# Performance work log

Measured on AMD Instinct MI355X. Metric: run time of the kernel, lower is better.

The kernel has to match this reference:

```python
import jax, jax.numpy as jnp
import numpy as np

D_MODEL = 1024
NUM_HEADS = 16
D_K = D_MODEL // NUM_HEADS


def setup_inputs() -> dict:
    key = jax.random.key(0)
    ks = jax.random.split(key, 9)
    B, S = 2, 2048
    s_in = 1.0 / np.sqrt(D_MODEL)
    x = jax.random.normal(ks[0], (B, S, D_MODEL), dtype=jnp.float32)
    # Linear weights stored as (in_features, out_features): y = x @ W + b
    Wq = jax.random.uniform(ks[1], (D_MODEL, D_MODEL), jnp.float32, -s_in, s_in)
    bq = jax.random.uniform(ks[2], (D_MODEL,), jnp.float32, -s_in, s_in)
    Wk = jax.random.uniform(ks[3], (D_MODEL, D_K), jnp.float32, -s_in, s_in)
    bk = jax.random.uniform(ks[4], (D_K,), jnp.float32, -s_in, s_in)
    Wv = jax.random.uniform(ks[5], (D_MODEL, D_K), jnp.float32, -s_in, s_in)
    bv = jax.random.uniform(ks[6], (D_K,), jnp.float32, -s_in, s_in)
    Wo = jax.random.uniform(ks[7], (D_MODEL, D_MODEL), jnp.float32, -s_in, s_in)
    bo = jax.random.uniform(ks[8], (D_MODEL,), jnp.float32, -s_in, s_in)
    return {"x": x, "Wq": Wq, "bq": bq, "Wk": Wk, "bk": bk,
            "Wv": Wv, "bv": bv, "Wo": Wo, "bo": bo}


def reference(x, Wq, bq, Wk, bk, Wv, bv, Wo, bo):
    B, S, _ = x.shape
    H, Dk = NUM_HEADS, D_K
    # Projections
    Q = (x @ Wq + bq).reshape(B, S, H, Dk).transpose(0, 2, 1, 3)  # [B,H,S,Dk]
    K = x @ Wk + bk                                               # [B,S,Dk] single KV head
    V = x @ Wv + bv                                               # [B,S,Dk]
    # Scores: query heads broadcast against the single shared KV head
    scores = jnp.einsum('bhqd,bkd->bhqk', Q, K) / jnp.sqrt(jnp.float32(Dk))
    attn = jax.nn.softmax(scores, axis=-1)                        # [B,H,S,S]
    out = jnp.einsum('bhqk,bkd->bhqd', attn, V)                   # [B,H,S,Dk]
    out = out.transpose(0, 2, 1, 3).reshape(B, S, H * Dk)         # [B,S,d_model]
    return out @ Wo + bo
```

## Files before the change

kernel.cpp:

```cpp
#include <hip/hip_runtime.h>
#include <hip/hip_bf16.h>

typedef __attribute__((ext_vector_type(8))) short bf16x8;
typedef __attribute__((ext_vector_type(4))) float f32x4;
typedef __attribute__((ext_vector_type(16))) float f32x16;
typedef __attribute__((ext_vector_type(4))) unsigned short ushort4v;

#define QSCALE 0.1803368801111204f

__device__ __forceinline__ unsigned short f2bf(float f) {
  union { float f; unsigned int u; } x; x.f = f;
  unsigned int u = x.u;
  unsigned int r = (u + 0x7fffu + ((u >> 16) & 1u)) >> 16;
  return (unsigned short)r;
}

__device__ __forceinline__ void gll16(const unsigned short* g, unsigned short* l) {
  __builtin_amdgcn_global_load_lds(
      (const __attribute__((address_space(1))) unsigned int*)g,
      (__attribute__((address_space(3))) unsigned int*)l, 16, 0, 0);
}

__global__ __launch_bounds__(256) void prep_kernel(
    const float* __restrict__ x,
    const float* __restrict__ Wq, const float* __restrict__ Wk,
    const float* __restrict__ Wv, const float* __restrict__ Wo,
    unsigned short* __restrict__ xb,
    unsigned short* __restrict__ QKVt, unsigned short* __restrict__ Wot) {
  int z = blockIdx.z;
  if (z == 4) {
    size_t base = ((size_t)(blockIdx.y * 32 + blockIdx.x)) * 4096 + threadIdx.x * 16;
#pragma unroll
    for (int c = 0; c < 4; ++c) {
      float4 v = *(const float4*)(x + base + c * 4);
      ushort4v o = { f2bf(v.x), f2bf(v.y), f2bf(v.z), f2bf(v.w) };
      *(ushort4v*)(xb + base + c * 4) = o;
    }
    return;
  }
  __shared__ float t[32][33];
  const float* src;
  unsigned short* dst;
  int C, rowoff;
  if (z == 0)      { src = Wq; dst = QKVt; C = 1024; rowoff = 0; }
  else if (z == 1) { src = Wk; dst = QKVt; C = 64;   rowoff = 1024; }
  else if (z == 2) { src = Wv; dst = QKVt; C = 64;   rowoff = 1088; }
  else             { src = Wo; dst = Wot;  C = 1024; rowoff = 0; }
  int c0 = blockIdx.x * 32, r0 = blockIdx.y * 32;
  if (c0 >= C) return;
  int tx = threadIdx.x & 31, ty = threadIdx.x >> 5;
#pragma unroll
  for (int i = 0; i < 32; i += 8)
    t[ty + i][tx] = src[(size_t)(r0 + ty + i) * C + c0 + tx];
  __syncthreads();
#pragma unroll
  for (int i = 0; i < 32; i += 8)
    dst[(size_t)(rowoff + c0 + ty + i) * 1024 + r0 + tx] = f2bf(t[tx][ty + i]);
}

template <typename OutT, bool QKVMODE>
__global__ __launch_bounds__(256, 4) void gemm_bf16_kernel(
    const unsigned short* __restrict__ A, const unsigned short* __restrict__ Bt,
    const float* __restrict__ b0, const float* __restrict__ b1,
    const float* __restrict__ b2, OutT* __restrict__ C,
    unsigned short* __restrict__ Vt, int M, int N, int K) {
  __shared__ __align__(16) unsigned short As[2][64 * 32];
  __shared__ __align__(16) unsigned short Bs[2][64 * 32];
  int tid = threadIdx.x;
  int wid = tid >> 6, lane = tid & 63;
  int l15 = lane & 15, quad = lane >> 4;
  int m0 = blockIdx.x * 64, n0 = blockIdx.y * 64;
  int mw = (wid >> 1) * 32, nw = (wid & 1) * 32;
  f32x4 acc[2][2];
#pragma unroll
  for (int i = 0; i < 2; i++)
#pragma unroll
    for (int j = 0; j < 2; j++)
#pragma unroll
      for (int e = 0; e < 4; ++e) acc[i][j][e] = 0.f;

  int u = tid;
  int srow = u >> 2;
  int gq = (u & 3) ^ ((srow >> 1) & 3);
  const unsigned short* Ag = A + (size_t)(m0 + srow) * K + gq * 8;
  const unsigned short* Bg = Bt + (size_t)(n0 + srow) * K + gq * 8;

  gll16(Ag, As[0] + u * 8);
  gll16(Bg, Bs[0] + u * 8);

  for (int k0 = 0; k0 < K; k0 += 32) {
    int cur = (k0 >> 5) & 1;
    if (k0 + 32 < K) {
      int nxt = cur ^ 1;
      gll16(Ag + k0 + 32, As[nxt] + u * 8);
      gll16(Bg + k0 + 32, Bs[nxt] + u * 8);
      asm volatile("s_waitcnt vmcnt(2)" ::: "memory");
    } else {
      asm volatile("s_waitcnt vmcnt(0)" ::: "memory");
    }
    __builtin_amdgcn_s_barrier();
    __builtin_amdgcn_sched_barrier(0);
    const unsigned short* Asb = As[cur];
    const unsigned short* Bsb = Bs[cur];
    bf16x8 af[2], bfr[2];
#pragma unroll
    for (int t = 0; t < 2; ++t) {
      int row = mw + t * 16 + l15;
      af[t] = *(const bf16x8*)(Asb + row * 32 + ((quad ^ ((row >> 1) & 3)) * 8));
    }
#pragma unroll
    for (int t = 0; t < 2; ++t) {
      int row = nw + t * 16 + l15;
      bfr[t] = *(const bf16x8*)(Bsb + row * 32 + ((quad ^ ((row >> 1) & 3)) * 8));
    }
#pragma unroll
    for (int mt = 0; mt < 2; ++mt)
#pragma unroll
      for (int nt = 0; nt < 2; ++nt)
        acc[mt][nt] = __builtin_amdgcn_mfma_f32_16x16x32_bf16(
            af[mt], bfr[nt], acc[mt][nt], 0, 0, 0);
    asm volatile("s_waitcnt lgkmcnt(0)" ::: "memory");
    __builtin_amdgcn_sched_barrier(0);
    __builtin_amdgcn_s_barrier();
  }
#pragma unroll
  for (int mt = 0; mt < 2; ++mt)
#pragma unroll
    for (int nt = 0; nt < 2; ++nt) {
      int col = n0 + nw + nt * 16 + l15;
      float bias, cs;
      if constexpr (QKVMODE) {
        bias = (col < 1024) ? b0[col] : ((col < 1088) ? b1[col - 1024] : b2[col - 1088]);
        cs = (col < 1024) ? QSCALE : 1.0f;
      } else {
        bias = b0[col];
        cs = 1.0f;
      }
#pragma unroll
      for (int r = 0; r < 4; ++r) {
        int row = m0 + mw + mt * 16 + quad * 4 + r;
        float v = (acc[mt][nt][r] + bias) * cs;
        if constexpr (sizeof(OutT) == 2)
          C[(size_t)row * N + col] = f2bf(v);
        else
          C[(size_t)row * N + col] = v;
        if constexpr (QKVMODE) {
          if (col >= 1088)
            Vt[((size_t)(row >> 11) * 64 + (col - 1088)) * 2048 + (row & 2047)] =
                f2bf(v);
        }
      }
    }
}

__global__ __launch_bounds__(512, 4) void flash_attn_kernel(
    const unsigned short* __restrict__ QKV,
    const unsigned short* __restrict__ Vt,
    unsigned short* __restrict__ AO) {
  constexpr int S = 2048, LDQ = 1152;
  constexpr int PK = 72;
  __shared__ __align__(16) unsigned short smem[2][2][64 * PK];
  int tid = threadIdx.x;
  int wid = tid >> 6, lane = tid & 63;
  int l31 = lane & 31, half = lane >> 5;
  int p = wid & 3, ks = wid >> 2;
  int q0 = blockIdx.x * 128, h = blockIdx.y, b = blockIdx.z;

  const unsigned short* Qb =
      QKV + (size_t)(b * S + q0 + p * 32 + l31) * LDQ + h * 64 + half * 8;
  bf16x8 qf[4];
#pragma unroll
  for (int f = 0; f < 4; ++f) qf[f] = *(const bf16x8*)(Qb + f * 16);

  int u = tid & 255, sl = tid >> 8;
  int srow = u >> 2, sc = (u & 3) * 8;
  const unsigned short* Kgb = QKV + ((size_t)b * S) * LDQ + 1024;
  const unsigned short* Vgb = Vt + ((size_t)(b * 64 + srow)) * 2048;

  f32x16 oa0, oa1;
#pragma unroll
  for (int r = 0; r < 16; ++r) { oa0[r] = 0.f; oa1[r] = 0.f; }
  float rs = 0.f;

  int kb0 = sl * 1024;
  bf16x8 ka = *(const bf16x8*)(Kgb + (size_t)(kb0 + srow) * LDQ + sc);
  bf16x8 kc = *(const bf16x8*)(Kgb + (size_t)(kb0 + srow) * LDQ + sc + 32);
  bf16x8 va = *(const bf16x8*)(Vgb + kb0 + sc);
  bf16x8 vc = *(const bf16x8*)(Vgb + kb0 + sc + 32);

  unsigned short* Ksb = smem[ks][0];
  unsigned short* Vsb = smem[ks][1];

  for (int kt = 0; kt < 16; ++kt) {
    *(bf16x8*)(smem[sl][0] + srow * PK + sc) = ka;
    *(bf16x8*)(smem[sl][0] + srow * PK + sc + 32) = kc;
    *(bf16x8*)(smem[sl][1] + srow * PK + sc) = va;
    *(bf16x8*)(smem[sl][1] + srow * PK + sc + 32) = vc;
    __syncthreads();
    if (kt + 1 < 16) {
      int kbn = sl * 1024 + (kt + 1) * 64;
      ka = *(const bf16x8*)(Kgb + (size_t)(kbn + srow) * LDQ + sc);
      kc = *(const bf16x8*)(Kgb + (size_t)(kbn + srow) * LDQ + sc + 32);
      va = *(const bf16x8*)(Vgb + kbn + sc);
      vc = *(const bf16x8*)(Vgb + kbn + sc + 32);
    }

#pragma unroll
    for (int n2 = 0; n2 < 2; ++n2) {
      f32x16 sacc;
#pragma unroll
      for (int i = 0; i < 16; ++i) sacc[i] = 0.f;
#pragma unroll
      for (int s = 0; s < 4; ++s) {
        bf16x8 kf =
            *(const bf16x8*)(Ksb + (n2 * 32 + l31) * PK + s * 16 + half * 8);
        sacc = __builtin_amdgcn_mfma_f32_32x32x16_bf16(kf, qf[s], sacc, 0, 0, 0);
      }
#pragma unroll
      for (int t = 0; t < 2; ++t) {
        float pr[8];
#pragma unroll
        for (int j = 0; j < 8; ++j) {
          pr[j] = __builtin_amdgcn_exp2f(sacc[t * 8 + j]);
          rs += pr[j];
        }
        unsigned w0A, w1A, w0B, w1B;
        asm("v_cvt_pk_bf16_f32 %0, %1, %2" : "=v"(w0A) : "v"(pr[0]), "v"(pr[1]));
        asm("v_cvt_pk_bf16_f32 %0, %1, %2" : "=v"(w1A) : "v"(pr[2]), "v"(pr[3]));
        asm("v_cvt_pk_bf16_f32 %0, %1, %2" : "=v"(w0B) : "v"(pr[4]), "v"(pr[5]));
        asm("v_cvt_pk_bf16_f32 %0, %1, %2" : "=v"(w1B) : "v"(pr[6]), "v"(pr[7]));
        asm volatile("v_permlane32_swap_b32 %0, %1" : "+v"(w0A), "+v"(w0B));
        asm volatile("v_permlane32_swap_b32 %0, %1" : "+v"(w1A), "+v"(w1B));
        union { unsigned u[4]; bf16x8 v; } afu;
        afu.u[0] = w0A; afu.u[1] = w1A; afu.u[2] = w0B; afu.u[3] = w1B;
        int sg = n2 * 2 + t;
        bf16x8 vf0 = *(const bf16x8*)(Vsb + (l31) * PK + sg * 16 + half * 8);
        bf16x8 vf1 = *(const bf16x8*)(Vsb + (32 + l31) * PK + sg * 16 + half * 8);
        oa0 = __builtin_amdgcn_mfma_f32_32x32x16_bf16(afu.v, vf0, oa0, 0, 0, 0);
        oa1 = __builtin_amdgcn_mfma_f32_32x32x16_bf16(afu.v, vf1, oa1, 0, 0, 0);
      }
    }
    __syncthreads();
  }

  float rsf = rs + __shfl_xor(rs, 32, 64);

  float* Cb = (float*)smem;
  if (ks == 1) {
#pragma unroll
    for (int r = 0; r < 16; ++r) {
      int row = (r & 3) + 8 * (r >> 2) + 4 * half;
      Cb[(p * 32 + row) * 66 + l31] = oa0[r];
      Cb[(p * 32 + row) * 66 + 32 + l31] = oa1[r];
    }
    if (half == 0) Cb[(p * 32 + l31) * 66 + 64] = rsf;
  } else {
    if (half == 0) Cb[(p * 32 + l31) * 66 + 65] = rsf;
  }
  __syncthreads();
  if (ks == 0) {
    unsigned short* Ob = AO + (size_t)(b * S + q0 + p * 32) * 1024 + h * 64;
#pragma unroll
    for (int r = 0; r < 16; ++r) {
      int row = (r & 3) + 8 * (r >> 2) + 4 * half;
      float p0 = Cb[(p * 32 + row) * 66 + l31];
      float p1 = Cb[(p * 32 + row) * 66 + 32 + l31];
      float inv = 1.0f / (Cb[(p * 32 + row) * 66 + 64] + Cb[(p * 32 + row) * 66 + 65]);
      Ob[(size_t)row * 1024 + l31] = f2bf((oa0[r] + p0) * inv);
      Ob[(size_t)row * 1024 + 32 + l31] = f2bf((oa1[r] + p1) * inv);
    }
  }
}

extern "C" void kernel_launch(void* const* d_in, const int* in_sizes, int n_in,
                              void* d_out, int out_size, void* d_ws, size_t ws_size,
                              hipStream_t stream) {
  const float* x  = (const float*)d_in[0];
  const float* Wq = (const float*)d_in[1];
  const float* bq = (const float*)d_in[2];
  const float* Wk = (const float*)d_in[3];
  const float* bk = (const float*)d_in[4];
  const float* Wv = (const float*)d_in[5];
  const float* bv = (const float*)d_in[6];
  const float* Wo = (const float*)d_in[7];
  const float* bo = (const float*)d_in[8];
  float* out = (float*)d_out;

  constexpr int B = 2, S = 2048, D = 1024, Dk = 64, H = 16;
  constexpr int M = B * S;
  constexpr int NQKV = D + 2 * Dk;

  char* ws = (char*)d_ws;
  unsigned short* xb   = (unsigned short*)ws; ws += (size_t)M * D * 2;
  unsigned short* QKVt = (unsigned short*)ws; ws += (size_t)NQKV * D * 2;
  unsigned short* Wot  = (unsigned short*)ws; ws += (size_t)D * D * 2;
  unsigned short* QKV  = (unsigned short*)ws; ws += (size_t)M * NQKV * 2;
  unsigned short* Vtb  = (unsigned short*)ws; ws += (size_t)B * Dk * S * 2;
  unsigned short* AO   = (unsigned short*)ws; ws += (size_t)M * D * 2;

  prep_kernel<<<dim3(32, 32, 5), 256, 0, stream>>>(x, Wq, Wk, Wv, Wo, xb, QKVt, Wot);

  gemm_bf16_kernel<unsigned short, true><<<dim3(M / 64, NQKV / 64), 256, 0, stream>>>(
      xb, QKVt, bq, bk, bv, QKV, Vtb, M, NQKV, D);

  flash_attn_kernel<<<dim3(S / 128, H, B), 512, 0, stream>>>(QKV, Vtb, AO);

  gemm_bf16_kernel<float, false><<<dim3(M / 64, D / 64), 256, 0, stream>>>(
      AO, Wot, bo, nullptr, nullptr, out, nullptr, M, D, D);
}
```

Before: 168.4 us.

## Fuse fp32-to-bf16 conversion of x into QKV GEMM A-tile loading

Removes the separate x→bf16 conversion pass from the prep kernel. The QKV GEMM now loads fp32 x tiles into registers, converts them with v_cvt_pk_bf16_f32 and writes them to LDS, while B still uses direct global-to-LDS loads. This saves writing and re-reading the 8 MB bf16 copy of x. The cost is that the GEMM reads twice the A bytes (fp32), repeated across the 18 N-tile blocks, and the A path becomes a register-staged pipeline with a different wait/barrier structure.

```diff
diff --git a/kernel.cpp b/kernel.cpp
--- a/kernel.cpp
+++ b/kernel.cpp
@@ -22,22 +22,10 @@
 }
 
 __global__ __launch_bounds__(256) void prep_kernel(
-    const float* __restrict__ x,
     const float* __restrict__ Wq, const float* __restrict__ Wk,
     const float* __restrict__ Wv, const float* __restrict__ Wo,
-    unsigned short* __restrict__ xb,
     unsigned short* __restrict__ QKVt, unsigned short* __restrict__ Wot) {
   int z = blockIdx.z;
-  if (z == 4) {
-    size_t base = ((size_t)(blockIdx.y * 32 + blockIdx.x)) * 4096 + threadIdx.x * 16;
-#pragma unroll
-    for (int c = 0; c < 4; ++c) {
-      float4 v = *(const float4*)(x + base + c * 4);
-      ushort4v o = { f2bf(v.x), f2bf(v.y), f2bf(v.z), f2bf(v.w) };
-      *(ushort4v*)(xb + base + c * 4) = o;
-    }
-    return;
-  }
   __shared__ float t[32][33];
   const float* src;
   unsigned short* dst;
@@ -58,9 +46,9 @@
     dst[(size_t)(rowoff + c0 + ty + i) * 1024 + r0 + tx] = f2bf(t[tx][ty + i]);
 }
 
-template <typename OutT, bool QKVMODE>
+template <typename OutT, bool QKVMODE, bool FP32A>
 __global__ __launch_bounds__(256, 4) void gemm_bf16_kernel(
-    const unsigned short* __restrict__ A, const unsigned short* __restrict__ Bt,
+    const void* __restrict__ Av, const unsigned short* __restrict__ Bt,
     const float* __restrict__ b0, const float* __restrict__ b1,
     const float* __restrict__ b2, OutT* __restrict__ C,
     unsigned short* __restrict__ Vt, int M, int N, int K) {
@@ -82,24 +70,51 @@
   int u = tid;
   int srow = u >> 2;
   int gq = (u & 3) ^ ((srow >> 1) & 3);
-  const unsigned short* Ag = A + (size_t)(m0 + srow) * K + gq * 8;
+  const unsigned short* A16 = (const unsigned short*)Av;
+  const float* A32 = (const float*)Av;
+  const unsigned short* Ag = A16 + (size_t)(m0 + srow) * K + gq * 8;
+  const float* Ag32 = A32 + (size_t)(m0 + srow) * K + gq * 8;
   const unsigned short* Bg = Bt + (size_t)(n0 + srow) * K + gq * 8;
 
-  gll16(Ag, As[0] + u * 8);
+  float4 aC0, aC1;
   gll16(Bg, Bs[0] + u * 8);
+  if constexpr (FP32A) {
+    aC0 = *(const float4*)(Ag32);
+    aC1 = *(const float4*)(Ag32 + 4);
+  } else {
+    gll16(Ag, As[0] + u * 8);
+  }
 
   for (int k0 = 0; k0 < K; k0 += 32) {
     int cur = (k0 >> 5) & 1;
-    if (k0 + 32 < K) {
-      int nxt = cur ^ 1;
-      gll16(Ag + k0 + 32, As[nxt] + u * 8);
-      gll16(Bg + k0 + 32, Bs[nxt] + u * 8);
-      asm volatile("s_waitcnt vmcnt(2)" ::: "memory");
+    int nxt = cur ^ 1;
+    if constexpr (FP32A) {
+      union { unsigned w[4]; bf16x8 v; } cvt;
+      asm("v_cvt_pk_bf16_f32 %0, %1, %2" : "=v"(cvt.w[0]) : "v"(aC0.x), "v"(aC0.y));
+      asm("v_cvt_pk_bf16_f32 %0, %1, %2" : "=v"(cvt.w[1]) : "v"(aC0.z), "v"(aC0.w));
+      asm("v_cvt_pk_bf16_f32 %0, %1, %2" : "=v"(cvt.w[2]) : "v"(aC1.x), "v"(aC1.y));
+      asm("v_cvt_pk_bf16_f32 %0, %1, %2" : "=v"(cvt.w[3]) : "v"(aC1.z), "v"(aC1.w));
+      *(bf16x8*)(As[cur] + u * 8) = cvt.v;
+      if (k0 + 32 < K) {
+        gll16(Bg + k0 + 32, Bs[nxt] + u * 8);
+        aC0 = *(const float4*)(Ag32 + k0 + 32);
+        aC1 = *(const float4*)(Ag32 + k0 + 36);
+      }
+      asm volatile("s_waitcnt lgkmcnt(0)" ::: "memory");
+      __builtin_amdgcn_sched_barrier(0);
+      __builtin_amdgcn_s_barrier();
+      __builtin_amdgcn_sched_barrier(0);
     } else {
-      asm volatile("s_waitcnt vmcnt(0)" ::: "memory");
-    }
-    __builtin_amdgcn_s_barrier();
-    __builtin_amdgcn_sched_barrier(0);
+      if (k0 + 32 < K) {
+        gll16(Ag + k0 + 32, As[nxt] + u * 8);
+        gll16(Bg + k0 + 32, Bs[nxt] + u * 8);
+        asm volatile("s_waitcnt vmcnt(2)" ::: "memory");
+      } else {
+        asm volatile("s_waitcnt vmcnt(0)" ::: "memory");
+      }
+      __builtin_amdgcn_s_barrier();
+      __builtin_amdgcn_sched_barrier(0);
+    }
     const unsigned short* Asb = As[cur];
     const unsigned short* Bsb = Bs[cur];
     bf16x8 af[2], bfr[2];
@@ -291,20 +306,19 @@
   constexpr int NQKV = D + 2 * Dk;
 
   char* ws = (char*)d_ws;
-  unsigned short* xb   = (unsigned short*)ws; ws += (size_t)M * D * 2;
   unsigned short* QKVt = (unsigned short*)ws; ws += (size_t)NQKV * D * 2;
   unsigned short* Wot  = (unsigned short*)ws; ws += (size_t)D * D * 2;
   unsigned short* QKV  = (unsigned short*)ws; ws += (size_t)M * NQKV * 2;
   unsigned short* Vtb  = (unsigned short*)ws; ws += (size_t)B * Dk * S * 2;
   unsigned short* AO   = (unsigned short*)ws; ws += (size_t)M * D * 2;
 
-  prep_kernel<<<dim3(32, 32, 5), 256, 0, stream>>>(x, Wq, Wk, Wv, Wo, xb, QKVt, Wot);
-
-  gemm_bf16_kernel<unsigned short, true><<<dim3(M / 64, NQKV / 64), 256, 0, stream>>>(
-      xb, QKVt, bq, bk, bv, QKV, Vtb, M, NQKV, D);
+  prep_kernel<<<dim3(32, 32, 4), 256, 0, stream>>>(Wq, Wk, Wv, Wo, QKVt, Wot);
+
+  gemm_bf16_kernel<unsigned short, true, true><<<dim3(M / 64, NQKV / 64), 256, 0, stream>>>(
+      x, QKVt, bq, bk, bv, QKV, Vtb, M, NQKV, D);
 
   flash_attn_kernel<<<dim3(S / 128, H, B), 512, 0, stream>>>(QKV, Vtb, AO);
 
-  gemm_bf16_kernel<float, false><<<dim3(M / 64, D / 64), 256, 0, stream>>>(
+  gemm_bf16_kernel<float, false, false><<<dim3(M / 64, D / 64), 256, 0, stream>>>(
       AO, Wot, bo, nullptr, nullptr, out, nullptr, M, D, D);
 }
```

Measured after the change: 173.9 us. 3.3% more time.
